# Kernel tuning notes

Measured on AMD Instinct MI355X. Metric: run time of the kernel, lower is better.

Reference implementation:

```python
import jax, jax.numpy as jnp
import numpy as np

N_EXPERTS = 8
TOP_K = 2

def setup_inputs() -> dict:
    key = jax.random.key(0)
    ks = jax.random.split(key, 7)
    d, h, e = 1024, 4096, N_EXPERTS
    x = jax.random.normal(ks[0], (4, 2048, d), dtype=jnp.float32)
    gate_w = jax.random.normal(ks[1], (d, e), dtype=jnp.float32) * (1.0 / np.sqrt(d))
    gate_b = jnp.zeros((e,), dtype=jnp.float32)
    w1 = jax.random.normal(ks[2], (e, d, h), dtype=jnp.float32) * (1.0 / np.sqrt(d))
    b1 = jnp.zeros((e, h), dtype=jnp.float32)
    w2 = jax.random.normal(ks[3], (e, h, d), dtype=jnp.float32) * (1.0 / np.sqrt(h))
    b2 = jnp.zeros((e, d), dtype=jnp.float32)
    return {"x": x, "gate_w": gate_w, "gate_b": gate_b,
            "w1": w1, "b1": b1, "w2": w2, "b2": b2}

def reference(x, gate_w, gate_b, w1, b1, w2, b2):
    B, T, C = x.shape
    xf = x.reshape(-1, C)                                  # [N, C]
    gate_logits = xf @ gate_w + gate_b                     # [N, E]
    top_vals, top_idx = jax.lax.top_k(gate_logits, TOP_K)  # [N, K]
    top_w = jax.nn.softmax(top_vals, axis=-1)              # softmax over selected logits
    out = jnp.zeros_like(xf)
    for i in range(N_EXPERTS):
        # per-token combine weight for expert i (0 if not in top-k)
        wi = jnp.sum(jnp.where(top_idx == i, top_w, 0.0), axis=-1)  # [N]
        h = jax.nn.gelu(xf @ w1[i] + b1[i], approximate=False)      # [N, 4C]
        y = h @ w2[i] + b2[i]                                       # [N, C]
        out = out + wi[:, None] * y
    return out.reshape(B, T, C)
```

## Files before the change

kernel.cpp:

```cpp
#include <hip/hip_runtime.h>
#include <math.h>


#define NTOK 8192
#define CDIM 1024
#define HDIM 4096
#define NEXP 8
#define MAXT2 71
#define MAXROWS2 (MAXT2 * 256)

typedef unsigned short u16;
typedef __attribute__((ext_vector_type(8))) _Float16 half8;
typedef __attribute__((ext_vector_type(4))) float f32x4;

__device__ __forceinline__ u16 f2h(float f) {
    union { _Float16 h; u16 u; } cv; cv.h = (_Float16)f; return cv.u;
}
__device__ __forceinline__ void gll16(const u16* g, u16* l) {
    __builtin_amdgcn_global_load_lds((__attribute__((address_space(1))) void*)(g),
                                     (__attribute__((address_space(3))) void*)(l),
                                     16, 0, 0);
}
__device__ __forceinline__ float gelu_f(float v) {
    float u = 0.70710678118654752f * v;
    float au = fabsf(u);
    float t = __builtin_amdgcn_rcpf(1.0f + 0.3275911f * au);
    float p = t * (0.254829592f + t * (-0.284496736f + t * (1.421413741f +
              t * (-1.453152027f + t * 1.061405429f))));
    float ea = __expf(-au * au);
    float er = 1.0f - p * ea;
    er = (u < 0.f) ? -er : er;
    return 0.5f * v * (1.0f + er);
}
__device__ __forceinline__ int xcd_remap(int lid, int nact) {
    int q = nact >> 3, r = nact & 7;
    int xcd = lid & 7, pos = lid >> 3;
    return (xcd < r) ? (xcd * (q + 1) + pos) : (r * (q + 1) + (xcd - r) * q + pos);
}
__device__ __forceinline__ int sched_nt(const int* __restrict__ cnt8) {
    int at = 0;
#pragma unroll
    for (int q = 0; q < NEXP; ++q) at += (cnt8[q] + 255) >> 8;
    return at;
}
__device__ __forceinline__ void sched_tile(const int* __restrict__ cnt8, int t,
                                           int& e, int& rt, int& prow, int& cnte) {
    int at = 0, ar = 0; e = -1; rt = 0; prow = 0; cnte = 0;
#pragma unroll
    for (int q = 0; q < NEXP; ++q) {
        int c = cnt8[q]; int ti = (c + 255) >> 8;
        if (e < 0 && t < at + ti) { e = q; rt = t - at; prow = ar; cnte = c; }
        at += ti; ar += ti * 256;
    }
}

__device__ __forceinline__ void route_body(
    int blk, const float* __restrict__ x, const float* __restrict__ gw,
    const float* __restrict__ gb, u16* __restrict__ xh,
    float2* __restrict__ rtw, int* __restrict__ choice)
{
    int tid = threadIdx.x, lane = tid & 63, wid = tid >> 6;
    int tok = blk * 4 + wid;
    const float* xr = x + (size_t)tok * CDIM;
    float a[NEXP];
#pragma unroll
    for (int e = 0; e < NEXP; e++) a[e] = 0.f;
#pragma unroll
    for (int j = 0; j < 4; j++) {
        int k0 = j * 256 + lane * 4;
        float4 xv = *reinterpret_cast<const float4*>(xr + k0);
        ushort4 hv;
        hv.x = f2h(xv.x); hv.y = f2h(xv.y); hv.z = f2h(xv.z); hv.w = f2h(xv.w);
        *reinterpret_cast<ushort4*>(xh + (size_t)tok * CDIM + k0) = hv;
        const float* gr = gw + (size_t)k0 * NEXP;
#pragma unroll
        for (int t = 0; t < 4; t++) {
            float xs = (t == 0) ? xv.x : (t == 1) ? xv.y : (t == 2) ? xv.z : xv.w;
            float4 g0 = *reinterpret_cast<const float4*>(gr + t * 8);
            float4 g1 = *reinterpret_cast<const float4*>(gr + t * 8 + 4);
            a[0] += xs * g0.x; a[1] += xs * g0.y; a[2] += xs * g0.z; a[3] += xs * g0.w;
            a[4] += xs * g1.x; a[5] += xs * g1.y; a[6] += xs * g1.z; a[7] += xs * g1.w;
        }
    }
#pragma unroll
    for (int ofs = 32; ofs >= 1; ofs >>= 1) {
#pragma unroll
        for (int e = 0; e < NEXP; e++) a[e] += __shfl_xor(a[e], ofs, 64);
    }
    if (lane == 0) {
#pragma unroll
        for (int e = 0; e < NEXP; e++) a[e] += gb[e];
        int i0 = 0; float v0 = a[0];
#pragma unroll
        for (int e = 1; e < NEXP; e++) if (a[e] > v0) { v0 = a[e]; i0 = e; }
        int i1 = -1; float v1 = -3.4e38f;
#pragma unroll
        for (int e = 0; e < NEXP; e++) if (e != i0 && a[e] > v1) { v1 = a[e]; i1 = e; }
        float t = expf(v1 - v0);
        float w0 = 1.f / (1.f + t);
        rtw[tok] = make_float2(w0, t * w0);
        choice[tok] = i0 | (i1 << 4);
    }
}

__device__ __forceinline__ void transpose_body4(
    int bx, int by, int e, const float* __restrict__ src, u16* __restrict__ dst,
    int R, int S, u16* tile)
{
    const float* se = src + (size_t)e * R * S;
    u16* de = dst + (size_t)e * R * S;
    int c0 = bx * 256, r0 = by * 64;
    int tid = threadIdx.x;
    int bc = tid & 15, br = tid >> 4;
    int wr = tid & 15, cr = tid >> 4;
#pragma unroll
    for (int q = 0; q < 4; ++q) {
        int cq = c0 + q * 64;
        u16 h[4][4];
#pragma unroll
        for (int i = 0; i < 4; i++) {
            float4 v = *reinterpret_cast<const float4*>(
                se + (size_t)(r0 + 4 * br + i) * S + cq + 4 * bc);
            h[i][0] = f2h(v.x); h[i][1] = f2h(v.y); h[i][2] = f2h(v.z); h[i][3] = f2h(v.w);
        }
        if (q) __syncthreads();
#pragma unroll
        for (int j = 0; j < 4; j++) {
            ushort4 w;
            w.x = h[0][j]; w.y = h[1][j]; w.z = h[2][j]; w.w = h[3][j];
            int row = 4 * bc + j;
            *reinterpret_cast<ushort4*>(&tile[row * 64 + ((br ^ (row & 15)) << 2)]) = w;
        }
        __syncthreads();
#pragma unroll
        for (int i = 0; i < 4; i++) {
            int row = cr + 16 * i;
            ushort4 o = *reinterpret_cast<const ushort4*>(
                &tile[row * 64 + ((wr ^ (row & 15)) << 2)]);
            *reinterpret_cast<ushort4*>(de + (size_t)(cq + row) * R + r0 + 4 * wr) = o;
        }
    }
}

__global__ __launch_bounds__(256) void k_prep(
    const float* __restrict__ x, const float* __restrict__ gw,
    const float* __restrict__ gb, u16* __restrict__ xh,
    float2* __restrict__ rtw, int* __restrict__ choice,
    const float* __restrict__ w1, u16* __restrict__ w1t,
    const float* __restrict__ w2, u16* __restrict__ w2t)
{
    __shared__ __align__(16) u16 tile[64 * 64];
    int z = blockIdx.z;
    int bxf = blockIdx.x;
    if (z == 0) {
        route_body(bxf, x, gw, gb, xh, rtw, choice);
    } else if (z == 1) {
        int e = bxf >> 8, r = bxf & 255;
        transpose_body4(r & 15, r >> 4, e, w1, w1t, CDIM, HDIM, tile);
    } else {
        int e = bxf >> 8, r = bxf & 255;
        transpose_body4(r & 3, r >> 2, e, w2, w2t, HDIM, CDIM, tile);
    }
}

__global__ __launch_bounds__(256) void k_lists(
    const int* __restrict__ choice, int* __restrict__ cnt, int* __restrict__ lists)
{
    __shared__ int wsum[4];
    __shared__ int base;
    int e = blockIdx.x;
    int tid = threadIdx.x, lane = tid & 63, wv = tid >> 6;
    if (tid == 0) base = 0;
    __syncthreads();
    for (int t0 = 0; t0 < NTOK; t0 += 256) {
        int tok = t0 + tid;
        int ch = choice[tok];
        int i0 = ch & 15, i1 = (ch >> 4) & 15;
        int pred = (i0 == e || i1 == e) ? 1 : 0;
        int entry = tok * 2 + ((i0 == e) ? 0 : 1);
        unsigned long long m = __ballot(pred);
        int wpre = __popcll(m & ((1ull << lane) - 1ull));
        if (lane == 0) wsum[wv] = __popcll(m);
        __syncthreads();
        int pre = wpre;
#pragma unroll
        for (int w2 = 0; w2 < 4; ++w2) if (w2 < wv) pre += wsum[w2];
        int tot = wsum[0] + wsum[1] + wsum[2] + wsum[3];
        if (pred) lists[e * NTOK + base + pre] = entry;
        __syncthreads();
        if (tid == 0) base += tot;
        __syncthreads();
    }
    if (tid == 0) cnt[e] = base;
}

#define DSA(BUF, QR) do { \
    _Pragma("unroll") for (int fm_ = 0; fm_ < 4; ++fm_) { \
        af[fm_][0] = HA[aIdx0 + ((QR) * 4 + fm_) * 128 + (BUF) * 2048]; \
        af[fm_][1] = HA[aIdx1 + ((QR) * 4 + fm_) * 128 + (BUF) * 2048]; \
    } } while (0)

#define DSB(BUF, QC) do { \
    _Pragma("unroll") for (int fn_ = 0; fn_ < 2; ++fn_) { \
        bf[QC][fn_][0] = HB[bIdx0 + ((QC) * 2 + fn_) * 128 + (BUF) * 2048]; \
        bf[QC][fn_][1] = HB[bIdx1 + ((QC) * 2 + fn_) * 128 + (BUF) * 2048]; \
    } } while (0)

#define FFN_MFMA(QR, QC) do { \
    __builtin_amdgcn_s_setprio(1); \
    _Pragma("unroll") for (int fm_ = 0; fm_ < 4; ++fm_) \
    _Pragma("unroll") for (int fn_ = 0; fn_ < 2; ++fn_) { \
        acc[(QR) * 4 + fm_][(QC) * 2 + fn_] = __builtin_amdgcn_mfma_f32_16x16x32_f16( \
            bf[QC][fn_][0], af[fm_][0], acc[(QR) * 4 + fm_][(QC) * 2 + fn_], 0, 0, 0); \
        acc[(QR) * 4 + fm_][(QC) * 2 + fn_] = __builtin_amdgcn_mfma_f32_16x16x32_f16( \
            bf[QC][fn_][1], af[fm_][1], acc[(QR) * 4 + fm_][(QC) * 2 + fn_], 0, 0, 0); \
    } \
    __builtin_amdgcn_s_setprio(0); } while (0)

#define PUB()  __builtin_amdgcn_s_barrier()
#define PUBG() do { __builtin_amdgcn_s_barrier(); \
                    __builtin_amdgcn_sched_barrier(0); } while (0)
#define VMW4() asm volatile("s_waitcnt vmcnt(4)" ::: "memory")

#define STA(BUF, H) do { \
    gll16(pa[H][0], ldsA + (BUF) * 16384 + ((H) * 128 + wv * 16) * 64); pa[H][0] += 64; \
    gll16(pa[H][1], ldsA + (BUF) * 16384 + ((H) * 128 + wv * 16 + 8) * 64); pa[H][1] += 64; } while (0)

#define STB(BUF, H) do { \
    gll16(pb[H][0], ldsB + (BUF) * 16384 + ((H) * 128 + wv * 16) * 64); pb[H][0] += 64; \
    gll16(pb[H][1], ldsB + (BUF) * 16384 + ((H) * 128 + wv * 16 + 8) * 64); pb[H][1] += 64; } while (0)

#define FFN_KLOOP(NK) do { \
    STB(0, 0); STB(0, 1); STA(0, 0); STA(0, 1); STB(1, 0); STB(1, 1); \
    VMW4(); PUBG(); \
    for (int i_ = 0; i_ < (NK) / 2; ++i_) { \
        DSA(0, 0); DSB(0, 0); STA(1, 0);  PUB(); FFN_MFMA(0, 0); PUB(); \
        DSB(0, 1); STA(1, 1);             PUB(); FFN_MFMA(0, 1); PUBG(); \
        DSA(0, 1); STB(0, 0);             PUB(); FFN_MFMA(1, 0); PUB(); \
        STB(0, 1); VMW4();                PUB(); FFN_MFMA(1, 1); PUBG(); \
        DSA(1, 0); DSB(1, 0); STA(0, 0);  PUB(); FFN_MFMA(0, 0); PUB(); \
        DSB(1, 1); STA(0, 1);             PUB(); FFN_MFMA(0, 1); PUBG(); \
        DSA(1, 1); STB(1, 0);             PUB(); FFN_MFMA(1, 0); PUB(); \
        STB(1, 1); VMW4();                PUB(); FFN_MFMA(1, 1); PUBG(); \
    } } while (0)

__global__ __launch_bounds__(512, 2) void k_ffn1(
    const u16* __restrict__ xh, const u16* __restrict__ w1t,
    const float* __restrict__ b1, u16* __restrict__ hbuf,
    const int* __restrict__ ctrl, const int* __restrict__ lists)
{
    extern __shared__ __align__(16) u16 lds[];
    u16* ldsA = lds;
    u16* ldsB = lds + 2 * 256 * 64;
    const half8* HA = reinterpret_cast<const half8*>(ldsA);
    const half8* HB = reinterpret_cast<const half8*>(ldsB);
    const int* cnt8 = ctrl + 8;
    int lid = blockIdx.y * gridDim.x + blockIdx.x;
    int nt = sched_nt(cnt8);
    int nact = nt * 16;
    if (lid >= nact) return;
    int w = xcd_remap(lid, nact);
    int nt8 = nt * 8;
    int byh = w / nt8;
    int rem = w - byh * nt8;
    int t = rem >> 3;
    int by = byh * 8 + (rem & 7);
    int e, rt, prow, cnte;
    sched_tile(cnt8, t, e, rt, prow, cnte);
    int n0 = by * 256;
    int tid = threadIdx.x, lane = tid & 63, wv = tid >> 6;
    int wm = wv >> 2, wn = wv & 3;
    int lr = lane >> 3;
    int chunk = (lane & 7) ^ lr;
    const int* lrow = lists + e * NTOK + rt * 256;
    int first_ent = lists[e * NTOK];
    const u16* pa[2][2]; const u16* pb[2][2];
#pragma unroll
    for (int h = 0; h < 2; ++h)
#pragma unroll
        for (int g = 0; g < 2; ++g) {
            int r = h * 128 + wv * 16 + g * 8 + lr;
            int ent = (rt * 256 + r < cnte) ? lrow[r] : first_ent;
            int tok = ent >> 1;
            pa[h][g] = xh + (size_t)tok * CDIM + chunk * 8;
            pb[h][g] = w1t + (size_t)e * HDIM * CDIM + (size_t)(n0 + r) * CDIM + chunk * 8;
        }
    int aIdx0 = wm * 1024 + (lane & 15) * 8 + ((lane >> 4) ^ (lane & 7));
    int aIdx1 = wm * 1024 + (lane & 15) * 8 + (((lane >> 4) + 4) ^ (lane & 7));
    int bIdx0 = wn * 512 + (lane & 15) * 8 + ((lane >> 4) ^ (lane & 7));
    int bIdx1 = wn * 512 + (lane & 15) * 8 + (((lane >> 4) + 4) ^ (lane & 7));
    f32x4 acc[8][4];
#pragma unroll
    for (int m = 0; m < 8; ++m)
#pragma unroll
        for (int n = 0; n < 4; ++n) acc[m][n] = f32x4{0.f, 0.f, 0.f, 0.f};
    half8 af[4][2], bf[2][2][2];

    FFN_KLOOP(16);

    const f32x4* b1v = reinterpret_cast<const f32x4*>(b1 + (size_t)e * HDIM);
    f32x4 bv[4];
#pragma unroll
    for (int n = 0; n < 4; ++n)
        bv[n] = b1v[(n0 + wn * 64 + n * 16) / 4 + (lane >> 4)];
#pragma unroll
    for (int m = 0; m < 8; ++m) {
        int grow = prow + rt * 256 + wm * 128 + m * 16 + (lane & 15);
        u16* hr = hbuf + (size_t)grow * HDIM + n0 + wn * 64 + (lane >> 4) * 4;
#pragma unroll
        for (int n = 0; n < 4; ++n) {
            ushort4 o;
#pragma unroll
            for (int j = 0; j < 4; ++j)
                ((u16*)&o)[j] = f2h(gelu_f(acc[m][n][j] + bv[n][j]));
            *reinterpret_cast<ushort4*>(hr + n * 16) = o;
        }
    }
}

__global__ __launch_bounds__(512, 2) void k_ffn2(
    const u16* __restrict__ hbuf, const u16* __restrict__ w2t,
    const float* __restrict__ b2, float* __restrict__ ybuf,
    const int* __restrict__ ctrl, const int* __restrict__ lists,
    const float2* __restrict__ rtw)
{
    extern __shared__ __align__(16) u16 lds[];
    u16* ldsA = lds;
    u16* ldsB = lds + 2 * 256 * 64;
    const half8* HA = reinterpret_cast<const half8*>(ldsA);
    const half8* HB = reinterpret_cast<const half8*>(ldsB);
    const int* cnt8 = ctrl + 8;
    int lid = ((int)blockIdx.z * gridDim.y + blockIdx.y) * gridDim.x + blockIdx.x;
    int nt = sched_nt(cnt8);
    int nact = nt * 8;
    if (lid >= nact) return;
    int w = xcd_remap(lid, nact);
    int nt4 = nt * 4;
    int kh = w / nt4;
    int rem = w - kh * nt4;
    int t = rem >> 2;
    int by = rem & 3;
    int e, rt, prow, cnte;
    sched_tile(cnt8, t, e, rt, prow, cnte);
    int n0 = by * 256;
    int tid = threadIdx.x, lane = tid & 63, wv = tid >> 6;
    int wm = wv >> 2, wn = wv & 3;
    int lr = lane >> 3;
    int chunk = (lane & 7) ^ lr;
    int rowbase = prow + rt * 256;
    const u16* pa[2][2]; const u16* pb[2][2];
#pragma unroll
    for (int h = 0; h < 2; ++h)
#pragma unroll
        for (int g = 0; g < 2; ++g) {
            int r = h * 128 + wv * 16 + g * 8 + lr;
            pa[h][g] = hbuf + (size_t)(rowbase + r) * HDIM + kh * 2048 + chunk * 8;
            pb[h][g] = w2t + (size_t)e * CDIM * HDIM + (size_t)(n0 + r) * HDIM + kh * 2048 + chunk * 8;
        }
    int aIdx0 = wm * 1024 + (lane & 15) * 8 + ((lane >> 4) ^ (lane & 7));
    int aIdx1 = wm * 1024 + (lane & 15) * 8 + (((lane >> 4) + 4) ^ (lane & 7));
    int bIdx0 = wn * 512 + (lane & 15) * 8 + ((lane >> 4) ^ (lane & 7));
    int bIdx1 = wn * 512 + (lane & 15) * 8 + (((lane >> 4) + 4) ^ (lane & 7));
    f32x4 acc[8][4];
#pragma unroll
    for (int m = 0; m < 8; ++m)
#pragma unroll
        for (int n = 0; n < 4; ++n) acc[m][n] = f32x4{0.f, 0.f, 0.f, 0.f};
    half8 af[4][2], bf[2][2][2];

    FFN_KLOOP(32);

    const f32x4* b2v = reinterpret_cast<const f32x4*>(b2 + (size_t)e * CDIM);
    f32x4 bv[4];
#pragma unroll
    for (int n = 0; n < 4; ++n)
        bv[n] = b2v[(n0 + wn * 64 + n * 16) / 4 + (lane >> 4)];
    const int* lrow = lists + e * NTOK;
#pragma unroll
    for (int m = 0; m < 8; ++m) {
        int p = rt * 256 + wm * 128 + m * 16 + (lane & 15);
        bool valid = p < cnte;
        int entry = valid ? lrow[p] : 0;
        float2 wpair = rtw[entry >> 1];
        float wgt = (entry & 1) ? wpair.y : wpair.x;
        float* yb = ybuf + ((size_t)((entry & 1) * 2 + kh) * NTOK + (size_t)(entry >> 1)) * CDIM
                  + n0 + wn * 64 + (lane >> 4) * 4;
#pragma unroll
        for (int n = 0; n < 4; ++n) {
            f32x4 v = acc[m][n];
            if (kh == 0) v = v + bv[n];
            v = v * wgt;
            if (valid) *reinterpret_cast<f32x4*>(yb + n * 16) = v;
        }
    }
}

__global__ __launch_bounds__(256) void k_combine(
    const float* __restrict__ ybuf, float* __restrict__ out)
{
    size_t i = ((size_t)blockIdx.x * 256 + threadIdx.x) * 4;
    const size_t S = (size_t)NTOK * CDIM;
    f32x4 a = *reinterpret_cast<const f32x4*>(ybuf + i);
    f32x4 b = *reinterpret_cast<const f32x4*>(ybuf + S + i);
    f32x4 c = *reinterpret_cast<const f32x4*>(ybuf + 2 * S + i);
    f32x4 d = *reinterpret_cast<const f32x4*>(ybuf + 3 * S + i);
    *reinterpret_cast<f32x4*>(out + i) = (a + b) + (c + d);
}

extern "C" void kernel_launch(void* const* d_in, const int* in_sizes, int n_in,
                              void* d_out, int out_size, void* d_ws, size_t ws_size,
                              hipStream_t stream)
{
    const float* x  = (const float*)d_in[0];
    const float* gw = (const float*)d_in[1];
    const float* gb = (const float*)d_in[2];
    const float* w1 = (const float*)d_in[3];
    const float* b1 = (const float*)d_in[4];
    const float* w2 = (const float*)d_in[5];
    const float* b2 = (const float*)d_in[6];
    float* out = (float*)d_out;
    char* ws = (char*)d_ws;

    size_t off = 0;
    int*    ctrl  = (int*)(ws + off);    off += 4096;
    float2* rtw   = (float2*)(ws + off); off += (size_t)NTOK * 8;
    int*    choice= (int*)(ws + off);    off += (size_t)NTOK * 4;
    int*    lists = (int*)(ws + off);    off += (size_t)NEXP * NTOK * 4;
    u16*    xh    = (u16*)(ws + off);    off += (size_t)NTOK * CDIM * 2;
    u16*    w1t   = (u16*)(ws + off);    off += (size_t)NEXP * CDIM * HDIM * 2;
    u16*    w2t   = (u16*)(ws + off);    off += (size_t)NEXP * CDIM * HDIM * 2;
    u16*    hbuf  = (u16*)(ws + off);    off += (size_t)MAXROWS2 * HDIM * 2;
    float*  ybuf  = (float*)(ws + off);  off += (size_t)4 * NTOK * CDIM * 4;
    (void)ws_size; (void)in_sizes; (void)n_in; (void)out_size;

    hipFuncSetAttribute((const void*)k_ffn1, hipFuncAttributeMaxDynamicSharedMemorySize, 131072);
    hipFuncSetAttribute((const void*)k_ffn2, hipFuncAttributeMaxDynamicSharedMemorySize, 131072);

    k_prep<<<dim3(2048, 1, 3), 256, 0, stream>>>(x, gw, gb, xh, rtw, choice,
                                                 w1, w1t, w2, w2t);
    k_lists<<<dim3(NEXP), 256, 0, stream>>>(choice, ctrl + 8, lists);
    k_ffn1<<<dim3(MAXT2, HDIM / 256), 512, 131072, stream>>>(xh, w1t, b1, hbuf, ctrl, lists);
    k_ffn2<<<dim3(MAXT2, CDIM / 256, 2), 512, 131072, stream>>>(hbuf, w2t, b2, ybuf, ctrl, lists, rtw);
    k_combine<<<dim3(NTOK * CDIM / 1024), 256, 0, stream>>>(ybuf, out);
}
```

Measured before the change: 541.6 us.

## Move w2 transpose into ffn1 launch to overlap with first GEMM

The w2 fp32-to-fp16 transpose moves out of the prep kernel and into extra blocks appended to the ffn1 grid, so it runs alongside the first expert GEMM instead of serially before it. The ffn1 grid becomes 1D, with inactive GEMM tiles returning early and the trailing 512 blocks each doing two transpose tiles using halves of the LDS. This shortens the prep critical path. In exchange, the transpose blocks compete with the GEMM blocks for CU slots and memory bandwidth, and they run at the 512-thread, 128KB-LDS block shape.

After: 510.5 us. -5.7%, faster.

```diff
diff --git a/kernel.cpp b/kernel.cpp
--- a/kernel.cpp
+++ b/kernel.cpp
@@ -8,6 +8,8 @@
 #define NEXP 8
 #define MAXT2 71
 #define MAXROWS2 (MAXT2 * 256)
+#define G1BLK (MAXT2 * 16)
+#define TRBLK 512
 
 typedef unsigned short u16;
 typedef __attribute__((ext_vector_type(8))) _Float16 half8;
@@ -103,14 +105,13 @@
     }
 }
 
-__device__ __forceinline__ void transpose_body4(
+__device__ __forceinline__ void transpose_body4t(
     int bx, int by, int e, const float* __restrict__ src, u16* __restrict__ dst,
-    int R, int S, u16* tile)
+    int R, int S, u16* tile, int tid)
 {
     const float* se = src + (size_t)e * R * S;
     u16* de = dst + (size_t)e * R * S;
     int c0 = bx * 256, r0 = by * 64;
-    int tid = threadIdx.x;
     int bc = tid & 15, br = tid >> 4;
     int wr = tid & 15, cr = tid >> 4;
 #pragma unroll
@@ -146,20 +147,16 @@
     const float* __restrict__ x, const float* __restrict__ gw,
     const float* __restrict__ gb, u16* __restrict__ xh,
     float2* __restrict__ rtw, int* __restrict__ choice,
-    const float* __restrict__ w1, u16* __restrict__ w1t,
-    const float* __restrict__ w2, u16* __restrict__ w2t)
+    const float* __restrict__ w1, u16* __restrict__ w1t)
 {
     __shared__ __align__(16) u16 tile[64 * 64];
     int z = blockIdx.z;
     int bxf = blockIdx.x;
     if (z == 0) {
         route_body(bxf, x, gw, gb, xh, rtw, choice);
-    } else if (z == 1) {
-        int e = bxf >> 8, r = bxf & 255;
-        transpose_body4(r & 15, r >> 4, e, w1, w1t, CDIM, HDIM, tile);
     } else {
         int e = bxf >> 8, r = bxf & 255;
-        transpose_body4(r & 3, r >> 2, e, w2, w2t, HDIM, CDIM, tile);
+        transpose_body4t(r & 15, r >> 4, e, w1, w1t, CDIM, HDIM, tile, threadIdx.x);
     }
 }
 
@@ -247,15 +244,27 @@
 __global__ __launch_bounds__(512, 2) void k_ffn1(
     const u16* __restrict__ xh, const u16* __restrict__ w1t,
     const float* __restrict__ b1, u16* __restrict__ hbuf,
-    const int* __restrict__ ctrl, const int* __restrict__ lists)
+    const int* __restrict__ ctrl, const int* __restrict__ lists,
+    const float* __restrict__ w2, u16* __restrict__ w2t)
 {
     extern __shared__ __align__(16) u16 lds[];
+    int lid = blockIdx.x;
+    int tid = threadIdx.x;
+    if (lid >= G1BLK) {
+        int tlid = lid - G1BLK;
+        int e = tlid >> 6, by = tlid & 63;
+        int half = tid >> 8, t2 = tid & 255;
+        u16* mytile = lds + half * 4096;
+#pragma unroll
+        for (int c4 = 0; c4 < 2; ++c4)
+            transpose_body4t(half * 2 + c4, by, e, w2, w2t, HDIM, CDIM, mytile, t2);
+        return;
+    }
     u16* ldsA = lds;
     u16* ldsB = lds + 2 * 256 * 64;
     const half8* HA = reinterpret_cast<const half8*>(ldsA);
     const half8* HB = reinterpret_cast<const half8*>(ldsB);
     const int* cnt8 = ctrl + 8;
-    int lid = blockIdx.y * gridDim.x + blockIdx.x;
     int nt = sched_nt(cnt8);
     int nact = nt * 16;
     if (lid >= nact) return;
@@ -268,7 +277,7 @@
     int e, rt, prow, cnte;
     sched_tile(cnt8, t, e, rt, prow, cnte);
     int n0 = by * 256;
-    int tid = threadIdx.x, lane = tid & 63, wv = tid >> 6;
+    int lane = tid & 63, wv = tid >> 6;
     int wm = wv >> 2, wn = wv & 3;
     int lr = lane >> 3;
     int chunk = (lane & 7) ^ lr;
@@ -436,10 +445,10 @@
     hipFuncSetAttribute((const void*)k_ffn1, hipFuncAttributeMaxDynamicSharedMemorySize, 131072);
     hipFuncSetAttribute((const void*)k_ffn2, hipFuncAttributeMaxDynamicSharedMemorySize, 131072);
 
-    k_prep<<<dim3(2048, 1, 3), 256, 0, stream>>>(x, gw, gb, xh, rtw, choice,
-                                                 w1, w1t, w2, w2t);
+    k_prep<<<dim3(2048, 1, 2), 256, 0, stream>>>(x, gw, gb, xh, rtw, choice, w1, w1t);
     k_lists<<<dim3(NEXP), 256, 0, stream>>>(choice, ctrl + 8, lists);
-    k_ffn1<<<dim3(MAXT2, HDIM / 256), 512, 131072, stream>>>(xh, w1t, b1, hbuf, ctrl, lists);
+    k_ffn1<<<dim3(G1BLK + TRBLK), 512, 131072, stream>>>(xh, w1t, b1, hbuf, ctrl, lists,
+                                                         w2, w2t);
     k_ffn2<<<dim3(MAXT2, CDIM / 256, 2), 512, 131072, stream>>>(hbuf, w2t, b2, ybuf, ctrl, lists, rtw);
     k_combine<<<dim3(NTOK * CDIM / 1024), 256, 0, stream>>>(ybuf, out);
 }
```
